# Kernel tuning notes

Hardware: AMD Instinct MI355X
Metric: run time of the kernel (lower is better)

## Reference

```python
import jax, jax.numpy as jnp
import numpy as np

V = 12288      # HEALPix vertices (nside=32)
C_IN = 128
C_OUT = 128
K = 4          # Chebyshev polynomial degree
DEG = 9        # nnz per Laplacian row (8 neighbors + self)
B = 8
BN_EPS = 1e-5


def setup_inputs() -> dict:
    key = jax.random.key(0)
    kx, kc, kv, kw = jax.random.split(key, 4)
    x = jax.random.normal(kx, (B, V, C_IN), dtype=jnp.float32)
    # sparse Laplacian as COO edge list: 9 entries per row
    lap_rows = jnp.repeat(jnp.arange(V, dtype=jnp.int32), DEG)          # [E]
    lap_cols = jax.random.randint(kc, (V * DEG,), 0, V, dtype=jnp.int32)
    lap_vals = jax.random.normal(kv, (V * DEG,), dtype=jnp.float32) * 0.1
    # Chebyshev weight [Fin*K, Fout] (Fin-major, K-minor, matching [B,V,Fin,K] reshape)
    weight = jax.random.normal(kw, (C_IN * K, C_OUT), dtype=jnp.float32) * (1.0 / np.sqrt(C_IN * K))
    gamma = jnp.ones((C_OUT,), dtype=jnp.float32)
    beta = jnp.zeros((C_OUT,), dtype=jnp.float32)
    return {"x": x, "lap_rows": lap_rows, "lap_cols": lap_cols,
            "lap_vals": lap_vals, "weight": weight, "gamma": gamma, "beta": beta}


def reference(x, lap_rows, lap_cols, lap_vals, weight, gamma, beta):
    b, v, c = x.shape
    k = weight.shape[0] // c

    def spmm(y):
        # y: [B, V, C] -> L @ y along vertex dim
        y2 = y.transpose(1, 0, 2).reshape(v, b * c)                 # [V, B*C]
        g = lap_vals[:, None] * y2[lap_cols]                        # [E, B*C]
        out = jnp.zeros((v, b * c), dtype=y.dtype).at[lap_rows].add(g)
        return out.reshape(v, b, c).transpose(1, 0, 2)              # [B, V, C]

    # Chebyshev recursion: T0 = x, T1 = L x, Tk = 2 L T_{k-1} - T_{k-2}
    terms = [x]
    if k > 1:
        terms.append(spmm(x))
    for _ in range(2, k):
        terms.append(2.0 * spmm(terms[-1]) - terms[-2])
    xk = jnp.stack(terms, axis=-1)                                  # [B, V, C, K]
    conv = jnp.einsum('bvck,cko->bvo', xk.reshape(b, v, c, k),
                      weight.reshape(c, k, -1))                     # [B, V, Cout]

    # BatchNorm1d over [B, Cout, V]: stats over (batch, vertices) per channel
    h = conv.transpose(0, 2, 1)                                     # [B, Cout, V]
    mean = jnp.mean(h, axis=(0, 2), keepdims=True)
    var = jnp.var(h, axis=(0, 2), keepdims=True)
    hn = (h - mean) * jax.lax.rsqrt(var + BN_EPS)
    return hn * gamma[None, :, None] + beta[None, :, None]          # [B, Cout, V]
```

## Files before the change

### kernel.cpp

```cpp
#include <hip/hip_runtime.h>

#define NV    12288
#define CIN   128
#define COUT  128
#define DEG   9
#define NB    8
#define NROWS (NB * NV)
#define KTOT  512
#define BM    192

typedef unsigned short bfu;
typedef __attribute__((ext_vector_type(8))) short short8;
typedef __attribute__((ext_vector_type(4))) float floatx4;
typedef __attribute__((ext_vector_type(4))) unsigned short ushort4v;

__device__ __forceinline__ float bf2f(unsigned short u) {
    union { unsigned int i; float f; } x;
    x.i = ((unsigned int)u) << 16;
    return x.f;
}
__device__ __forceinline__ unsigned short f2bf(float f) {
    union { float f; unsigned int i; } x;
    x.f = f;
    unsigned int r = x.i + 0x7FFFu + ((x.i >> 16) & 1u);
    return (unsigned short)(r >> 16);
}
__device__ __forceinline__ void gload16(const void* g, void* l) {
    __builtin_amdgcn_global_load_lds(
        (const __attribute__((address_space(1))) unsigned int*)g,
        (__attribute__((address_space(3))) unsigned int*)l, 16, 0, 0);
}

__global__ __launch_bounds__(256)
void prep_kernel(const float* __restrict__ x, bfu* __restrict__ xb,
                 const float* __restrict__ W, bfu* __restrict__ Wt,
                 float* __restrict__ stats)
{
    const int blk = blockIdx.x;
    const int t   = threadIdx.x;
    if (blk < 6144) {
        const size_t i = ((size_t)blk * 256 + t) * 8;
        const float4 a = *reinterpret_cast<const float4*>(x + i);
        const float4 b = *reinterpret_cast<const float4*>(x + i + 4);
        short8 r;
        r[0] = (short)f2bf(a.x); r[1] = (short)f2bf(a.y);
        r[2] = (short)f2bf(a.z); r[3] = (short)f2bf(a.w);
        r[4] = (short)f2bf(b.x); r[5] = (short)f2bf(b.y);
        r[6] = (short)f2bf(b.z); r[7] = (short)f2bf(b.w);
        *reinterpret_cast<short8*>(xb + i) = r;
    } else if (blk < 6400) {
        const int i = (blk - 6144) * 256 + t;
        const int o = i >> 9;
        const int kap = i & 511;
        const int s = kap >> 7;
        const int c = kap & 127;
        Wt[i] = f2bf(W[(size_t)(c * 4 + s) * COUT + o]);
    } else {
        stats[t] = 0.f;
    }
}

__global__ __launch_bounds__(256)
void spmm_bf16(const bfu* __restrict__ src, const bfu* __restrict__ sub,
               bfu* __restrict__ outp, const int* __restrict__ cols,
               const float* __restrict__ vals)
{
    const int t  = threadIdx.x;
    const int b  = blockIdx.x & 7;
    const int vt = blockIdx.x >> 3;
    const int v  = vt * 16 + (t >> 4);
    const int c0 = (t & 15) * 8;

    int   ec[DEG];
    float ev[DEG];
#pragma unroll
    for (int e = 0; e < DEG; ++e) {
        ec[e] = cols[v * DEG + e];
        ev[e] = vals[v * DEG + e];
    }

    float acc[8];
#pragma unroll
    for (int j = 0; j < 8; ++j) acc[j] = 0.f;

    const size_t bbase = (size_t)b * NV * CIN;
#pragma unroll
    for (int e = 0; e < DEG; ++e) {
        const short8 s = *reinterpret_cast<const short8*>(
            src + bbase + (size_t)ec[e] * CIN + c0);
#pragma unroll
        for (int j = 0; j < 8; ++j)
            acc[j] = fmaf(ev[e], bf2f((unsigned short)s[j]), acc[j]);
    }

    if (sub != nullptr) {
        const short8 s0 = *reinterpret_cast<const short8*>(
            sub + bbase + (size_t)v * CIN + c0);
#pragma unroll
        for (int j = 0; j < 8; ++j)
            acc[j] = 2.f * acc[j] - bf2f((unsigned short)s0[j]);
    }

    short8 r;
#pragma unroll
    for (int j = 0; j < 8; ++j) r[j] = (short)f2bf(acc[j]);
    *reinterpret_cast<short8*>(outp + bbase + (size_t)v * CIN + c0) = r;
}

__global__ __launch_bounds__(256)
void gemm_mfma(const bfu* __restrict__ A0, const bfu* __restrict__ A1,
               const bfu* __restrict__ A2, const bfu* __restrict__ A3,
               const bfu* __restrict__ Wt, bfu* __restrict__ convT,
               float* __restrict__ gstats)
{
    extern __shared__ char smem[];

    const int t    = threadIdx.x;
    const int lane = t & 63;
    const int wid  = t >> 6;
    const int wr   = wid >> 1;
    const int wc   = wid & 1;
    const int rbase = blockIdx.x * BM;
    const int ck   = t & 7;

    floatx4 acc[6][4];
#pragma unroll
    for (int m = 0; m < 6; ++m)
#pragma unroll
        for (int n = 0; n < 4; ++n) acc[m][n] = (floatx4){0.f, 0.f, 0.f, 0.f};

    const bfu* segs[4] = {A0, A1, A2, A3};

#define STAGE(KT, BUF)                                                        \
    {                                                                         \
        const bfu* As_ = segs[(KT) >> 1];                                     \
        const int  cb_ = ((KT) & 1) * 64;                                     \
        _Pragma("unroll")                                                     \
        for (int p = 0; p < 6; ++p) {                                         \
            const int flat = p * 256 + t;                                     \
            const int rr   = flat >> 3;                                       \
            gload16(As_ + (size_t)(rbase + rr) * CIN + cb_                    \
                        + ((ck ^ (rr & 7)) << 3),                             \
                    smem + (BUF) * 24576 + flat * 16);                        \
        }                                                                     \
        _Pragma("unroll")                                                     \
        for (int p = 0; p < 4; ++p) {                                         \
            const int flat = p * 256 + t;                                     \
            const int nn   = flat >> 3;                                       \
            gload16(Wt + (size_t)nn * KTOT + (KT) * 64                        \
                       + ((ck ^ (nn & 7)) << 3),                              \
                    smem + 49152 + (BUF) * 16384 + flat * 16);                \
        }                                                                     \
    }

    STAGE(0, 0);
    asm volatile("s_waitcnt vmcnt(0)\n\ts_barrier" ::: "memory");

#pragma unroll
    for (int kt = 0; kt < 8; ++kt) {
        if (kt < 7) STAGE(kt + 1, (kt + 1) & 1);

        const char* abase = smem + (kt & 1) * 24576;
        const char* bbase = smem + 49152 + (kt & 1) * 16384;
#pragma unroll
        for (int ks = 0; ks < 2; ++ks) {
            const int chunk = ((ks * 4 + (lane >> 4)) ^ (lane & 7)) * 16;
            short8 a[6], b[4];
#pragma unroll
            for (int m = 0; m < 6; ++m)
                a[m] = *reinterpret_cast<const short8*>(
                    abase + (wr * 96 + m * 16 + (lane & 15)) * 128 + chunk);
#pragma unroll
            for (int n = 0; n < 4; ++n)
                b[n] = *reinterpret_cast<const short8*>(
                    bbase + (wc * 64 + n * 16 + (lane & 15)) * 128 + chunk);
#pragma unroll
            for (int m = 0; m < 6; ++m)
#pragma unroll
                for (int n = 0; n < 4; ++n)
                    acc[m][n] = __builtin_amdgcn_mfma_f32_16x16x32_bf16(
                        a[m], b[n], acc[m][n], 0, 0, 0);
        }
        if (kt < 7)
            asm volatile("s_waitcnt vmcnt(0)\n\ts_barrier" ::: "memory");
    }
#undef STAGE

    __syncthreads();
    float* sred = (float*)smem;
    float* qred = sred + COUT;
    if (t < COUT) { sred[t] = 0.f; qred[t] = 0.f; }
    __syncthreads();

    const int batch = rbase / NV;
    const int v0 = (rbase % NV) + wr * 96 + (lane >> 4) * 4;
    const int ob = wc * 64 + (lane & 15);

#pragma unroll
    for (int n = 0; n < 4; ++n) {
        const int o = ob + n * 16;
        float s = 0.f, q = 0.f;
        bfu* cbase = convT + ((size_t)batch * COUT + o) * NV + v0;
#pragma unroll
        for (int m = 0; m < 6; ++m) {
            const floatx4 v4 = acc[m][n];
            ushort4v r;
#pragma unroll
            for (int j = 0; j < 4; ++j) {
                r[j] = f2bf(v4[j]);
                s += v4[j];
                q = fmaf(v4[j], v4[j], q);
            }
            *reinterpret_cast<ushort4v*>(cbase + m * 16) = r;
        }
        s += __shfl_xor(s, 16); s += __shfl_xor(s, 32);
        q += __shfl_xor(q, 16); q += __shfl_xor(q, 32);
        if ((lane >> 4) == 0) {
            atomicAdd(&sred[o], s);
            atomicAdd(&qred[o], q);
        }
    }
    __syncthreads();
    if (t < COUT) {
        atomicAdd(&gstats[t], sred[t]);
        atomicAdd(&gstats[COUT + t], qred[t]);
    }
}

__global__ __launch_bounds__(256)
void normalize_bn(const bfu* __restrict__ convT, const float* __restrict__ stats,
                  const float* __restrict__ gamma, const float* __restrict__ beta,
                  float* __restrict__ outp)
{
    const size_t i = ((size_t)blockIdx.x * 256 + threadIdx.x) * 8;
    const int ch = (int)((i / NV) & (COUT - 1));
    const float invN = 1.0f / (float)NROWS;
    const float mean = stats[ch] * invN;
    const float var  = stats[COUT + ch] * invN - mean * mean;
    const float rsig = rsqrtf(var + 1e-5f);
    const float sc   = rsig * gamma[ch];
    const float sh   = beta[ch] - mean * sc;

    const short8 s = *reinterpret_cast<const short8*>(convT + i);
    float4 r0, r1;
    r0.x = fmaf(bf2f((unsigned short)s[0]), sc, sh);
    r0.y = fmaf(bf2f((unsigned short)s[1]), sc, sh);
    r0.z = fmaf(bf2f((unsigned short)s[2]), sc, sh);
    r0.w = fmaf(bf2f((unsigned short)s[3]), sc, sh);
    r1.x = fmaf(bf2f((unsigned short)s[4]), sc, sh);
    r1.y = fmaf(bf2f((unsigned short)s[5]), sc, sh);
    r1.z = fmaf(bf2f((unsigned short)s[6]), sc, sh);
    r1.w = fmaf(bf2f((unsigned short)s[7]), sc, sh);
    *reinterpret_cast<float4*>(outp + i)     = r0;
    *reinterpret_cast<float4*>(outp + i + 4) = r1;
}

extern "C" void kernel_launch(void* const* d_in, const int* in_sizes, int n_in,
                              void* d_out, int out_size, void* d_ws, size_t ws_size,
                              hipStream_t stream)
{
    (void)in_sizes; (void)n_in; (void)out_size; (void)ws_size;

    const float* x     = (const float*)d_in[0];
    const int*   cols  = (const int*)  d_in[2];
    const float* vals  = (const float*)d_in[3];
    const float* W     = (const float*)d_in[4];
    const float* gamma = (const float*)d_in[5];
    const float* beta  = (const float*)d_in[6];
    float*       out   = (float*)d_out;

    const size_t bufE = (size_t)NB * NV * CIN;

    bfu* xb    = (bfu*)d_ws;
    bfu* t1    = xb + bufE;
    bfu* t2    = t1 + bufE;
    bfu* t3    = t2 + bufE;
    bfu* convT = t3 + bufE;
    bfu* Wt    = convT + bufE;
    float* stats = (float*)(Wt + 65536);

    const dim3 blk(256);
    const int spmm_grid = (NV / 16) * NB;

    prep_kernel <<<6401, blk, 0, stream>>>(x, xb, W, Wt, stats);

    spmm_bf16 <<<spmm_grid, blk, 0, stream>>>(xb, nullptr, t1, cols, vals);
    spmm_bf16 <<<spmm_grid, blk, 0, stream>>>(t1, xb,      t2, cols, vals);
    spmm_bf16 <<<spmm_grid, blk, 0, stream>>>(t2, t1,      t3, cols, vals);

    gemm_mfma <<<NROWS / BM, blk, 81920, stream>>>(xb, t1, t2, t3, Wt, convT, stats);

    normalize_bn <<<NROWS * CIN / (256 * 8), blk, 0, stream>>>(
        convT, stats, gamma, beta, out);
}
```

Measured before the change: 119.4 us.

## Fuse BatchNorm normalization into GEMM via cooperative grid sync

Launches the MFMA GEMM as a cooperative kernel. Each block keeps its accumulators in registers, waits at a grid-wide barrier until the global channel statistics are complete, then writes normalized fp32 output directly. This removes the bf16 convT round trip through memory and the separate normalize launch. The costs are a grid barrier and the requirement that all 512 blocks, each with 80KB of LDS, be co-resident; if the cooperative launch fails, the code falls back to the old two-kernel path.

```diff
diff --git a/kernel.cpp b/kernel.cpp
--- a/kernel.cpp
+++ b/kernel.cpp
@@ -1,4 +1,7 @@
 #include <hip/hip_runtime.h>
+#include <hip/hip_cooperative_groups.h>
+
+namespace cg = cooperative_groups;
 
 #define NV    12288
 #define CIN   128
@@ -107,11 +110,13 @@
     *reinterpret_cast<short8*>(outp + bbase + (size_t)v * CIN + c0) = r;
 }
 
+template<bool COOP>
 __global__ __launch_bounds__(256)
 void gemm_mfma(const bfu* __restrict__ A0, const bfu* __restrict__ A1,
                const bfu* __restrict__ A2, const bfu* __restrict__ A3,
                const bfu* __restrict__ Wt, bfu* __restrict__ convT,
-               float* __restrict__ gstats)
+               float* __restrict__ gstats, const float* __restrict__ gamma,
+               const float* __restrict__ beta, float* __restrict__ outp)
 {
     extern __shared__ char smem[];
 
@@ -200,18 +205,14 @@
     for (int n = 0; n < 4; ++n) {
         const int o = ob + n * 16;
         float s = 0.f, q = 0.f;
-        bfu* cbase = convT + ((size_t)batch * COUT + o) * NV + v0;
 #pragma unroll
         for (int m = 0; m < 6; ++m) {
             const floatx4 v4 = acc[m][n];
-            ushort4v r;
 #pragma unroll
             for (int j = 0; j < 4; ++j) {
-                r[j] = f2bf(v4[j]);
                 s += v4[j];
                 q = fmaf(v4[j], v4[j], q);
             }
-            *reinterpret_cast<ushort4v*>(cbase + m * 16) = r;
         }
         s += __shfl_xor(s, 16); s += __shfl_xor(s, 32);
         q += __shfl_xor(q, 16); q += __shfl_xor(q, 32);
@@ -224,6 +225,44 @@
     if (t < COUT) {
         atomicAdd(&gstats[t], sred[t]);
         atomicAdd(&gstats[COUT + t], qred[t]);
+    }
+
+    if constexpr (COOP) {
+        cg::this_grid().sync();
+        const float invN = 1.0f / (float)NROWS;
+#pragma unroll
+        for (int n = 0; n < 4; ++n) {
+            const int o = ob + n * 16;
+            const float mean = gstats[o] * invN;
+            const float var  = gstats[COUT + o] * invN - mean * mean;
+            const float sc   = rsqrtf(var + 1e-5f) * gamma[o];
+            const float sh   = beta[o] - mean * sc;
+            float* obase = outp + ((size_t)batch * COUT + o) * NV + v0;
+#pragma unroll
+            for (int m = 0; m < 6; ++m) {
+                const floatx4 v4 = acc[m][n];
+                float4 r;
+                r.x = fmaf(v4[0], sc, sh);
+                r.y = fmaf(v4[1], sc, sh);
+                r.z = fmaf(v4[2], sc, sh);
+                r.w = fmaf(v4[3], sc, sh);
+                *reinterpret_cast<float4*>(obase + m * 16) = r;
+            }
+        }
+    } else {
+#pragma unroll
+        for (int n = 0; n < 4; ++n) {
+            const int o = ob + n * 16;
+            bfu* cbase = convT + ((size_t)batch * COUT + o) * NV + v0;
+#pragma unroll
+            for (int m = 0; m < 6; ++m) {
+                const floatx4 v4 = acc[m][n];
+                ushort4v r;
+#pragma unroll
+                for (int j = 0; j < 4; ++j) r[j] = f2bf(v4[j]);
+                *reinterpret_cast<ushort4v*>(cbase + m * 16) = r;
+            }
+        }
     }
 }
 
@@ -288,8 +327,23 @@
     spmm_bf16 <<<spmm_grid, blk, 0, stream>>>(t1, xb,      t2, cols, vals);
     spmm_bf16 <<<spmm_grid, blk, 0, stream>>>(t2, t1,      t3, cols, vals);
 
-    gemm_mfma <<<NROWS / BM, blk, 81920, stream>>>(xb, t1, t2, t3, Wt, convT, stats);
-
-    normalize_bn <<<NROWS * CIN / (256 * 8), blk, 0, stream>>>(
-        convT, stats, gamma, beta, out);
-}
+    {
+        const bfu *a0 = xb, *a1 = t1, *a2 = t2, *a3 = t3, *wt = Wt;
+        bfu* cv = convT;
+        float* st = stats;
+        const float *ga = gamma, *be = beta;
+        float* op = out;
+        void* args[] = {(void*)&a0, (void*)&a1, (void*)&a2, (void*)&a3,
+                        (void*)&wt, (void*)&cv, (void*)&st, (void*)&ga,
+                        (void*)&be, (void*)&op};
+        hipError_t err = hipLaunchCooperativeKernel(
+            (const void*)&gemm_mfma<true>, dim3(NROWS / BM), blk, args,
+            81920, stream);
+        if (err != hipSuccess) {
+            gemm_mfma<false><<<NROWS / BM, blk, 81920, stream>>>(
+                xb, t1, t2, t3, Wt, convT, stats, gamma, beta, out);
+            normalize_bn<<<NROWS * CIN / (256 * 8), blk, 0, stream>>>(
+                convT, stats, gamma, beta, out);
+        }
+    }
+}
```

Measured after the change: 165.3 us. 38.4% more time.
